# Performance work log

Hardware: AMD Instinct MI355X
Metric: run time of the kernel (lower is better)

## Reference

```python
import jax, jax.numpy as jnp
import numpy as np

QMAX = 32767.0   # 2**15 - 1
QMIN = -32768.0  # -2**15


def setup_inputs() -> dict:
    key = jax.random.key(0)
    k_x, k_w0, k_w1, k_s, k_b = jax.random.split(key, 5)
    N, Cin, Cout = 8192, 4096, 4096
    x = jax.random.normal(k_x, (N, Cin, 1, 1), dtype=jnp.float32)
    # Fake-quantized INT8 weights: build a fp32 weight, split into dual int8 planes
    # the same way prepare_from_weight does, so w0/w1 hold integer values in [-128,127].
    W = jax.random.normal(k_w0, (Cout, Cin), dtype=jnp.float32) * 0.02
    max_abs = jnp.maximum(jnp.max(jnp.abs(W), axis=1), 1e-8)
    s0 = max_abs / 127.0
    w0 = jnp.clip(jnp.round(W / s0[:, None]), -128.0, 127.0)
    R = W - s0[:, None] * w0
    max_abs_R = jnp.max(jnp.abs(R), axis=1)
    s1 = jnp.where(max_abs_R > 1e-3, max_abs_R / 127.0, 0.0)
    w1 = jnp.where((s1 > 0)[:, None],
                   jnp.clip(jnp.round(R / jnp.where(s1 > 0, s1, 1.0)[:, None]), -128.0, 127.0),
                   0.0)
    bias = jax.random.normal(k_b, (Cout,), dtype=jnp.float32) * 0.01
    return {"x": x, "w0": w0, "w1": w1, "s0": s0, "s1": s1, "bias": bias}


def reference(x, w0, w1, s0, s1, bias):
    N, Cin, H, W_ = x.shape  # H == W_ == 1
    x2d = x.reshape(N, Cin)
    # INT16 activation fake-quant with softplus-smoothed amax
    amax = jnp.max(jnp.abs(x2d), axis=1, keepdims=True)          # [N,1]
    scale_x = jax.nn.softplus(amax) / QMAX                       # [N,1]
    xq = jnp.clip(jnp.round(x2d / scale_x), QMIN, QMAX)          # [N,Cin]
    # dual 1x1 convs == two GEMMs: [N,Cin] x [Cin,Cout]
    y0 = jnp.einsum('nc,oc->no', xq, w0)
    y1 = jnp.einsum('nc,oc->no', xq, w1)
    y = (y0 * s0[None, :] + y1 * s1[None, :]) * scale_x + bias[None, :]
    return y.reshape(N, -1, 1, 1)
```

## Files before the change

### kernel.cpp

```cpp
#include <hip/hip_runtime.h>
#include <hip/hip_fp16.h>

#define N_ROWS 8192
#define K_DIM  4096
#define M_DIM  4096

typedef __attribute__((ext_vector_type(8))) _Float16 half8;
typedef __attribute__((ext_vector_type(4))) _Float16 half4v;
typedef __attribute__((ext_vector_type(4))) float    f32x4;

__global__ __launch_bounds__(256) void quant_kernel(
    const float* __restrict__ x, _Float16* __restrict__ xq, float* __restrict__ sx)
{
    const int row = blockIdx.x;
    const int t   = threadIdx.x;
    const float4* xr4 = (const float4*)(x + (size_t)row * K_DIM);

    float4 v[4];
    float am = 0.0f;
#pragma unroll
    for (int i = 0; i < 4; ++i) {
        v[i] = xr4[i * 256 + t];
        am = fmaxf(am, fmaxf(fmaxf(fabsf(v[i].x), fabsf(v[i].y)),
                             fmaxf(fabsf(v[i].z), fabsf(v[i].w))));
    }
#pragma unroll
    for (int off = 32; off; off >>= 1)
        am = fmaxf(am, __shfl_xor(am, off, 64));
    __shared__ float red[4];
    if ((t & 63) == 0) red[t >> 6] = am;
    __syncthreads();
    am = fmaxf(fmaxf(red[0], red[1]), fmaxf(red[2], red[3]));

    const float sp    = (am > 20.0f) ? am : log1pf(expf(am));
    const float scale = sp / 32767.0f;
    const float inv   = 32767.0f / sp;
    if (t == 0) sx[row] = scale;

    half4v* out4 = (half4v*)(xq + (size_t)row * K_DIM);
#pragma unroll
    for (int i = 0; i < 4; ++i) {
        float q0 = fminf(fmaxf(rintf(v[i].x * inv), -32768.0f), 32767.0f);
        float q1 = fminf(fmaxf(rintf(v[i].y * inv), -32768.0f), 32767.0f);
        float q2 = fminf(fmaxf(rintf(v[i].z * inv), -32768.0f), 32767.0f);
        float q3 = fminf(fmaxf(rintf(v[i].w * inv), -32768.0f), 32767.0f);
        half4v h;
        h[0] = (_Float16)q0; h[1] = (_Float16)q1;
        h[2] = (_Float16)q2; h[3] = (_Float16)q3;
        out4[i * 256 + t] = h;
    }
}

__global__ __launch_bounds__(256) void fold_kernel(
    const float* __restrict__ w0, const float* __restrict__ w1,
    const float* __restrict__ s0, const float* __restrict__ s1,
    _Float16* __restrict__ wp)
{
    const size_t gid  = (size_t)blockIdx.x * 256 + threadIdx.x;
    const size_t base = gid * 8;
    const int    o    = (int)(base >> 12);
    const float  a = s0[o], b = s1[o];

    const float4* p0 = (const float4*)(w0 + base);
    const float4* p1 = (const float4*)(w1 + base);
    float4 u0 = p0[0], u1 = p0[1];
    float4 v0 = p1[0], v1 = p1[1];

    half8 h;
    h[0] = (_Float16)(a * u0.x + b * v0.x);
    h[1] = (_Float16)(a * u0.y + b * v0.y);
    h[2] = (_Float16)(a * u0.z + b * v0.z);
    h[3] = (_Float16)(a * u0.w + b * v0.w);
    h[4] = (_Float16)(a * u1.x + b * v1.x);
    h[5] = (_Float16)(a * u1.y + b * v1.y);
    h[6] = (_Float16)(a * u1.z + b * v1.z);
    h[7] = (_Float16)(a * u1.w + b * v1.w);
    *(half8*)(wp + base) = h;
}

__device__ inline void async_load16(const void* g, void* l)
{
    __builtin_amdgcn_global_load_lds(
        (const __attribute__((address_space(1))) void*)g,
        (__attribute__((address_space(3))) void*)l, 16, 0, 0);
}

__global__ __launch_bounds__(256) void gemm_kernel(
    const _Float16* __restrict__ A,
    const _Float16* __restrict__ B,
    const float* __restrict__ sx,
    const float* __restrict__ bias,
    float* __restrict__ out)
{
    __shared__ __align__(16) _Float16 As[128 * 32];
    __shared__ __align__(16) _Float16 Bs[128 * 32];

    const int t    = threadIdx.x;
    const int wave = t >> 6;
    const int lane = t & 63;
    const int n0   = blockIdx.y * 128;
    const int o0   = blockIdx.x * 128;

    const int srow = lane >> 2;
    const int scol = (lane & 3) * 8;

    const int n_off = (wave >> 1) * 64;
    const int o_off = (wave & 1) * 64;

    const int fr = lane & 15;
    const int fk = (lane >> 4) * 8;

    f32x4 acc[4][4] = {};

    for (int kk = 0; kk < K_DIM; kk += 32) {
#pragma unroll
        for (int j = 0; j < 2; ++j) {
            const int row = j * 64 + wave * 16 + srow;
            async_load16(A + (size_t)(n0 + row) * K_DIM + kk + scol,
                         &As[row * 32 + scol]);
            async_load16(B + (size_t)(o0 + row) * K_DIM + kk + scol,
                         &Bs[row * 32 + scol]);
        }
        __syncthreads();

        half8 af[4], bf[4];
#pragma unroll
        for (int i = 0; i < 4; ++i)
            af[i] = *(const half8*)&As[(n_off + i * 16 + fr) * 32 + fk];
#pragma unroll
        for (int j = 0; j < 4; ++j)
            bf[j] = *(const half8*)&Bs[(o_off + j * 16 + fr) * 32 + fk];

#pragma unroll
        for (int i = 0; i < 4; ++i)
#pragma unroll
            for (int j = 0; j < 4; ++j)
                acc[i][j] = __builtin_amdgcn_mfma_f32_16x16x32_f16(
                    af[i], bf[j], acc[i][j], 0, 0, 0);

        __syncthreads();
    }

#pragma unroll
    for (int i = 0; i < 4; ++i) {
        const int nbase = n0 + n_off + i * 16 + (lane >> 4) * 4;
#pragma unroll
        for (int r = 0; r < 4; ++r) {
            const float s = sx[nbase + r];
            float* orow = out + (size_t)(nbase + r) * M_DIM;
#pragma unroll
            for (int j = 0; j < 4; ++j) {
                const int o = o0 + o_off + j * 16 + (lane & 15);
                orow[o] = acc[i][j][r] * s + bias[o];
            }
        }
    }
}

extern "C" void kernel_launch(void* const* d_in, const int* in_sizes, int n_in,
                              void* d_out, int out_size, void* d_ws, size_t ws_size,
                              hipStream_t stream)
{
    const float* x    = (const float*)d_in[0];
    const float* w0   = (const float*)d_in[1];
    const float* w1   = (const float*)d_in[2];
    const float* s0   = (const float*)d_in[3];
    const float* s1   = (const float*)d_in[4];
    const float* bias = (const float*)d_in[5];
    float* out = (float*)d_out;

    char* ws = (char*)d_ws;
    _Float16* xq = (_Float16*)ws;
    _Float16* wp = (_Float16*)(ws + (size_t)N_ROWS * K_DIM * 2);
    float*    sx = (float*)(ws + (size_t)N_ROWS * K_DIM * 2
                               + (size_t)M_DIM * K_DIM * 2);

    quant_kernel<<<N_ROWS, 256, 0, stream>>>(x, xq, sx);
    fold_kernel<<<(M_DIM * (size_t)K_DIM) / (256 * 8), 256, 0, stream>>>(w0, w1, s0, s1, wp);

    dim3 grid(M_DIM / 128, N_ROWS / 128);
    gemm_kernel<<<grid, 256, 0, stream>>>(xq, wp, sx, bias, out);
}
```

Baseline: 644.1 us.

## Merge prologue kernels, swizzle GEMM LDS columns, and group block order

Fuses the activation quantize and weight fold kernels into one launch that branches on block index. In the GEMM, the global-to-LDS load columns are XOR-swizzled and the fragment reads use the matching swizzle, to cut LDS bank conflicts on the half8 reads. The grid becomes 1D, with blocks grouped into 8x8 tile clusters so neighbouring blocks share A and B rows in cache. The swizzle keeps LDS addresses linear and permutes which global k-chunk lands in each slot, so its correctness depends on the global and LDS index mapping being inverted consistently.

```diff
diff --git a/kernel.cpp b/kernel.cpp
--- a/kernel.cpp
+++ b/kernel.cpp
@@ -9,73 +9,72 @@
 typedef __attribute__((ext_vector_type(4))) _Float16 half4v;
 typedef __attribute__((ext_vector_type(4))) float    f32x4;
 
-__global__ __launch_bounds__(256) void quant_kernel(
-    const float* __restrict__ x, _Float16* __restrict__ xq, float* __restrict__ sx)
-{
-    const int row = blockIdx.x;
-    const int t   = threadIdx.x;
-    const float4* xr4 = (const float4*)(x + (size_t)row * K_DIM);
-
-    float4 v[4];
-    float am = 0.0f;
-#pragma unroll
-    for (int i = 0; i < 4; ++i) {
-        v[i] = xr4[i * 256 + t];
-        am = fmaxf(am, fmaxf(fmaxf(fabsf(v[i].x), fabsf(v[i].y)),
-                             fmaxf(fabsf(v[i].z), fabsf(v[i].w))));
-    }
-#pragma unroll
-    for (int off = 32; off; off >>= 1)
-        am = fmaxf(am, __shfl_xor(am, off, 64));
-    __shared__ float red[4];
-    if ((t & 63) == 0) red[t >> 6] = am;
-    __syncthreads();
-    am = fmaxf(fmaxf(red[0], red[1]), fmaxf(red[2], red[3]));
-
-    const float sp    = (am > 20.0f) ? am : log1pf(expf(am));
-    const float scale = sp / 32767.0f;
-    const float inv   = 32767.0f / sp;
-    if (t == 0) sx[row] = scale;
-
-    half4v* out4 = (half4v*)(xq + (size_t)row * K_DIM);
-#pragma unroll
-    for (int i = 0; i < 4; ++i) {
-        float q0 = fminf(fmaxf(rintf(v[i].x * inv), -32768.0f), 32767.0f);
-        float q1 = fminf(fmaxf(rintf(v[i].y * inv), -32768.0f), 32767.0f);
-        float q2 = fminf(fmaxf(rintf(v[i].z * inv), -32768.0f), 32767.0f);
-        float q3 = fminf(fmaxf(rintf(v[i].w * inv), -32768.0f), 32767.0f);
-        half4v h;
-        h[0] = (_Float16)q0; h[1] = (_Float16)q1;
-        h[2] = (_Float16)q2; h[3] = (_Float16)q3;
-        out4[i * 256 + t] = h;
-    }
-}
-
-__global__ __launch_bounds__(256) void fold_kernel(
+__global__ __launch_bounds__(256) void prologue_kernel(
+    const float* __restrict__ x,  _Float16* __restrict__ xq, float* __restrict__ sx,
     const float* __restrict__ w0, const float* __restrict__ w1,
     const float* __restrict__ s0, const float* __restrict__ s1,
     _Float16* __restrict__ wp)
 {
-    const size_t gid  = (size_t)blockIdx.x * 256 + threadIdx.x;
-    const size_t base = gid * 8;
-    const int    o    = (int)(base >> 12);
-    const float  a = s0[o], b = s1[o];
+    const int t = threadIdx.x;
+    if (blockIdx.x < N_ROWS) {
+        const int row = blockIdx.x;
+        const float4* xr4 = (const float4*)(x + (size_t)row * K_DIM);
 
-    const float4* p0 = (const float4*)(w0 + base);
-    const float4* p1 = (const float4*)(w1 + base);
-    float4 u0 = p0[0], u1 = p0[1];
-    float4 v0 = p1[0], v1 = p1[1];
+        float4 v[4];
+        float am = 0.0f;
+#pragma unroll
+        for (int i = 0; i < 4; ++i) {
+            v[i] = xr4[i * 256 + t];
+            am = fmaxf(am, fmaxf(fmaxf(fabsf(v[i].x), fabsf(v[i].y)),
+                                 fmaxf(fabsf(v[i].z), fabsf(v[i].w))));
+        }
+#pragma unroll
+        for (int off = 32; off; off >>= 1)
+            am = fmaxf(am, __shfl_xor(am, off, 64));
+        __shared__ float red[4];
+        if ((t & 63) == 0) red[t >> 6] = am;
+        __syncthreads();
+        am = fmaxf(fmaxf(red[0], red[1]), fmaxf(red[2], red[3]));
 
-    half8 h;
-    h[0] = (_Float16)(a * u0.x + b * v0.x);
-    h[1] = (_Float16)(a * u0.y + b * v0.y);
-    h[2] = (_Float16)(a * u0.z + b * v0.z);
-    h[3] = (_Float16)(a * u0.w + b * v0.w);
-    h[4] = (_Float16)(a * u1.x + b * v1.x);
-    h[5] = (_Float16)(a * u1.y + b * v1.y);
-    h[6] = (_Float16)(a * u1.z + b * v1.z);
-    h[7] = (_Float16)(a * u1.w + b * v1.w);
-    *(half8*)(wp + base) = h;
+        const float sp    = (am > 20.0f) ? am : log1pf(expf(am));
+        const float scale = sp / 32767.0f;
+        const float inv   = 32767.0f / sp;
+        if (t == 0) sx[row] = scale;
+
+        half4v* out4 = (half4v*)(xq + (size_t)row * K_DIM);
+#pragma unroll
+        for (int i = 0; i < 4; ++i) {
+            float q0 = fminf(fmaxf(rintf(v[i].x * inv), -32768.0f), 32767.0f);
+            float q1 = fminf(fmaxf(rintf(v[i].y * inv), -32768.0f), 32767.0f);
+            float q2 = fminf(fmaxf(rintf(v[i].z * inv), -32768.0f), 32767.0f);
+            float q3 = fminf(fmaxf(rintf(v[i].w * inv), -32768.0f), 32767.0f);
+            half4v h;
+            h[0] = (_Float16)q0; h[1] = (_Float16)q1;
+            h[2] = (_Float16)q2; h[3] = (_Float16)q3;
+            out4[i * 256 + t] = h;
+        }
+    } else {
+        const size_t gid  = (size_t)(blockIdx.x - N_ROWS) * 256 + t;
+        const size_t base = gid * 8;
+        const int    o    = (int)(base >> 12);
+        const float  a = s0[o], b = s1[o];
+
+        const float4* p0 = (const float4*)(w0 + base);
+        const float4* p1 = (const float4*)(w1 + base);
+        float4 u0 = p0[0], u1 = p0[1];
+        float4 v0 = p1[0], v1 = p1[1];
+
+        half8 h;
+        h[0] = (_Float16)(a * u0.x + b * v0.x);
+        h[1] = (_Float16)(a * u0.y + b * v0.y);
+        h[2] = (_Float16)(a * u0.z + b * v0.z);
+        h[3] = (_Float16)(a * u0.w + b * v0.w);
+        h[4] = (_Float16)(a * u1.x + b * v1.x);
+        h[5] = (_Float16)(a * u1.y + b * v1.y);
+        h[6] = (_Float16)(a * u1.z + b * v1.z);
+        h[7] = (_Float16)(a * u1.w + b * v1.w);
+        *(half8*)(wp + base) = h;
+    }
 }
 
 __device__ inline void async_load16(const void* g, void* l)
@@ -98,17 +97,24 @@
     const int t    = threadIdx.x;
     const int wave = t >> 6;
     const int lane = t & 63;
-    const int n0   = blockIdx.y * 128;
-    const int o0   = blockIdx.x * 128;
+
+    const int tile = blockIdx.x >> 6;
+    const int loc  = blockIdx.x & 63;
+    const int o0   = ((tile & 3) * 8 + (loc & 7)) * 128;
+    const int n0   = ((tile >> 2) * 8 + (loc >> 3)) * 128;
 
     const int srow = lane >> 2;
-    const int scol = (lane & 3) * 8;
+    const int scl  = lane & 3;
+    const int scg  = scl ^ ((srow >> 1) & 3);
+    const int gcol = scg * 8;
+    const int lcol = scl * 8;
 
     const int n_off = (wave >> 1) * 64;
     const int o_off = (wave & 1) * 64;
 
     const int fr = lane & 15;
-    const int fk = (lane >> 4) * 8;
+    const int fg = lane >> 4;
+    const int fk = (fg ^ ((fr >> 1) & 3)) * 8;
 
     f32x4 acc[4][4] = {};
 
@@ -116,10 +122,10 @@
 #pragma unroll
         for (int j = 0; j < 2; ++j) {
             const int row = j * 64 + wave * 16 + srow;
-            async_load16(A + (size_t)(n0 + row) * K_DIM + kk + scol,
-                         &As[row * 32 + scol]);
-            async_load16(B + (size_t)(o0 + row) * K_DIM + kk + scol,
-                         &Bs[row * 32 + scol]);
+            async_load16(A + (size_t)(n0 + row) * K_DIM + kk + gcol,
+                         &As[row * 32 + lcol]);
+            async_load16(B + (size_t)(o0 + row) * K_DIM + kk + gcol,
+                         &Bs[row * 32 + lcol]);
         }
         __syncthreads();
 
@@ -175,9 +181,9 @@
     float*    sx = (float*)(ws + (size_t)N_ROWS * K_DIM * 2
                                + (size_t)M_DIM * K_DIM * 2);
 
-    quant_kernel<<<N_ROWS, 256, 0, stream>>>(x, xq, sx);
-    fold_kernel<<<(M_DIM * (size_t)K_DIM) / (256 * 8), 256, 0, stream>>>(w0, w1, s0, s1, wp);
+    prologue_kernel<<<N_ROWS + (M_DIM * K_DIM) / (256 * 8), 256, 0, stream>>>(
+        x, xq, sx, w0, w1, s0, s1, wp);
 
-    dim3 grid(M_DIM / 128, N_ROWS / 128);
-    gemm_kernel<<<grid, 256, 0, stream>>>(xq, wp, sx, bias, out);
+    gemm_kernel<<<(N_ROWS / 128) * (M_DIM / 128), 256, 0, stream>>>(
+        xq, wp, sx, bias, out);
 }
```

Measured after the change: 638.0 us. About the same (-0.9%).
